# Optimization experiments

Hardware: AMD Instinct MI355X
Metric: run time of the kernel (lower is better)

Reference implementation:

```python
import jax, jax.numpy as jnp
import numpy as np

LN_EPS = 1e-5

def _mha(xq, xkv, in_w, in_b, out_w, out_b, n_heads):
    # torch nn.MultiheadAttention, batch_first=True, dropout=0
    B, S, d = xq.shape
    T = xkv.shape[1]
    dh = d // n_heads
    wq, wk, wv = jnp.split(in_w, 3, axis=0)   # each [d, d]
    bq, bk, bv = jnp.split(in_b, 3)
    q = (xq @ wq.T + bq).reshape(B, S, n_heads, dh).transpose(0, 2, 1, 3)
    k = (xkv @ wk.T + bk).reshape(B, T, n_heads, dh).transpose(0, 2, 1, 3)
    v = (xkv @ wv.T + bv).reshape(B, T, n_heads, dh).transpose(0, 2, 1, 3)
    scores = jnp.einsum('bhsd,bhtd->bhst', q, k) / jnp.sqrt(jnp.asarray(dh, xq.dtype))
    attn = jax.nn.softmax(scores, axis=-1)    # explicit [B,H,S,T] weights (need_weights=True path)
    o = jnp.einsum('bhst,bhtd->bhsd', attn, v)
    o = o.transpose(0, 2, 1, 3).reshape(B, S, d)
    return o @ out_w.T + out_b

def _ln(x, g, b):
    mu = jnp.mean(x, axis=-1, keepdims=True)
    var = jnp.mean(jnp.square(x - mu), axis=-1, keepdims=True)
    return (x - mu) / jnp.sqrt(var + LN_EPS) * g + b

def setup_inputs() -> dict:
    key = jax.random.key(0)
    B, S, T, d, ff = 4, 1024, 1024, 1024, 4096
    ks = jax.random.split(key, 10)
    s = 0.02
    return {
        'x': jax.random.normal(ks[0], (B, S, d), jnp.float32),
        'mem': jax.random.normal(ks[1], (B, T, d), jnp.float32),
        'sa_in_w': jax.random.normal(ks[2], (3 * d, d), jnp.float32) * s,
        'sa_in_b': jnp.zeros((3 * d,), jnp.float32),
        'sa_out_w': jax.random.normal(ks[3], (d, d), jnp.float32) * s,
        'sa_out_b': jnp.zeros((d,), jnp.float32),
        'ca_in_w': jax.random.normal(ks[4], (3 * d, d), jnp.float32) * s,
        'ca_in_b': jnp.zeros((3 * d,), jnp.float32),
        'ca_out_w': jax.random.normal(ks[5], (d, d), jnp.float32) * s,
        'ca_out_b': jnp.zeros((d,), jnp.float32),
        'ff_w1': jax.random.normal(ks[6], (ff, d), jnp.float32) * s,
        'ff_b1': jnp.zeros((ff,), jnp.float32),
        'ff_w2': jax.random.normal(ks[7], (d, ff), jnp.float32) * s,
        'ff_b2': jnp.zeros((d,), jnp.float32),
        'ln1_g': jnp.ones((d,), jnp.float32), 'ln1_b': jnp.zeros((d,), jnp.float32),
        'ln2_g': jnp.ones((d,), jnp.float32), 'ln2_b': jnp.zeros((d,), jnp.float32),
        'ln3_g': jnp.ones((d,), jnp.float32), 'ln3_b': jnp.zeros((d,), jnp.float32),
        'n_heads': 16,
    }

def reference(x, mem, sa_in_w, sa_in_b, sa_out_w, sa_out_b,
              ca_in_w, ca_in_b, ca_out_w, ca_out_b,
              ff_w1, ff_b1, ff_w2, ff_b2,
              ln1_g, ln1_b, ln2_g, ln2_b, ln3_g, ln3_b, n_heads):
    sa = _mha(x, x, sa_in_w, sa_in_b, sa_out_w, sa_out_b, n_heads)
    x = _ln(x + sa, ln1_g, ln1_b)
    ca = _mha(x, mem, ca_in_w, ca_in_b, ca_out_w, ca_out_b, n_heads)
    x = _ln(x + ca, ln2_g, ln2_b)
    h = jax.nn.gelu(x @ ff_w1.T + ff_b1, approximate=False)  # torch nn.GELU default = exact erf
    ff = h @ ff_w2.T + ff_b2
    return _ln(x + ff, ln3_g, ln3_b)
```

## Files before the change

kernel.cpp:

```cpp
#include <hip/hip_runtime.h>
#include <cstddef>

#define D_MODEL 1024
#define SEQ     1024
#define BATCH   4
#define NHEAD   16
#define DH      64
#define FFDIM   4096
#define NTOK    (BATCH*SEQ)

typedef float f32x4  __attribute__((ext_vector_type(4)));
typedef short bf16x8 __attribute__((ext_vector_type(8)));

static __device__ __forceinline__ unsigned short f2bf(float x){
  union { float f; unsigned u; } v; v.f = x;
  unsigned r = v.u + 0x7fffu + ((v.u >> 16) & 1u);
  return (unsigned short)(r >> 16);
}

static __device__ __forceinline__ float bf2f(unsigned short h){
  union { unsigned u; float f; } v; v.u = ((unsigned)h) << 16; return v.f;
}

static __device__ __forceinline__ void gl_lds16(const void* g, void* l){
  __builtin_amdgcn_global_load_lds((const __attribute__((address_space(1))) void*)g,
                                   (__attribute__((address_space(3))) void*)l, 16, 0, 0);
}

struct CvtJobs {
  const float* src[8];
  unsigned short* dst[8];
  int n[8];
};

__global__ __launch_bounds__(256) void cvt_kernel(CvtJobs jobs){
  int seg = blockIdx.y;
  const float* s = jobs.src[seg];
  unsigned short* d = jobs.dst[seg];
  int n = jobs.n[seg];
  int stride = gridDim.x * 256 * 4;
  for (int i = (blockIdx.x*256 + threadIdx.x)*4; i < n; i += stride){
    float4 v = *(const float4*)(s + i);
    ushort4 o;
    o.x = f2bf(v.x); o.y = f2bf(v.y); o.z = f2bf(v.z); o.w = f2bf(v.w);
    *(ushort4*)(d + i) = o;
  }
}

template<int EPI>
static __device__ __forceinline__ void gemm_core(
    unsigned short* smem,
    const unsigned short* __restrict__ A,
    const unsigned short* __restrict__ B,
    const float* __restrict__ bias,
    void* __restrict__ out0,
    unsigned short* __restrict__ vt,
    int N, int K, int kbeg, int kend, int row0, int col0)
{
  unsigned short* As = smem;
  unsigned short* Bs = smem + 128*64;
  const int tid  = threadIdx.x;
  const int w    = tid >> 6, lane = tid & 63;
  const int quad = lane >> 4, l15 = lane & 15;
  const int lr   = lane >> 3, lc = lane & 7;
  const int csrc = lc ^ lr;
  const int sw   = l15 & 7;
  const int wm = (w >> 1) * 64, wn = (w & 1) * 64;

  f32x4 acc[4][4];
  const f32x4 zero4 = {0.f, 0.f, 0.f, 0.f};
  #pragma unroll
  for (int i=0;i<4;i++)
    #pragma unroll
    for (int j=0;j<4;j++)
      acc[i][j] = zero4;

  const unsigned short* Ag = A + (size_t)(row0 + lr)*K + csrc*8;
  const unsigned short* Bg = B + (size_t)(col0 + lr)*K + csrc*8;

  for (int k0 = kbeg; k0 < kend; k0 += 64){
    #pragma unroll
    for (int i=0;i<4;i++){
      gl_lds16(Ag + (size_t)(i*32 + w*8)*K + k0, &As[i*2048 + w*512]);
      gl_lds16(Bg + (size_t)(i*32 + w*8)*K + k0, &Bs[i*2048 + w*512]);
    }
    __syncthreads();
    #pragma unroll
    for (int ks=0; ks<2; ks++){
      bf16x8 af[4], bfr[4];
      #pragma unroll
      for (int i=0;i<4;i++)
        af[i] = *(const bf16x8*)&As[(wm + i*16 + l15)*64 + ((ks*4 + quad) ^ sw)*8];
      #pragma unroll
      for (int j=0;j<4;j++)
        bfr[j] = *(const bf16x8*)&Bs[(wn + j*16 + l15)*64 + ((ks*4 + quad) ^ sw)*8];
      #pragma unroll
      for (int i=0;i<4;i++)
        #pragma unroll
        for (int j=0;j<4;j++)
          acc[i][j] = __builtin_amdgcn_mfma_f32_16x16x32_bf16(af[i], bfr[j], acc[i][j], 0, 0, 0);
    }
    __syncthreads();
  }

  float bj[4];
  #pragma unroll
  for (int j=0;j<4;j++) bj[j] = bias[col0 + wn + j*16 + l15];

  #pragma unroll
  for (int i=0;i<4;i++){
    #pragma unroll
    for (int r=0;r<4;r++){
      int row = row0 + wm + i*16 + quad*4 + r;
      #pragma unroll
      for (int j=0;j<4;j++){
        int col = col0 + wn + j*16 + l15;
        float v = acc[i][j][r] + bj[j];
        if (EPI == 2){
          float t = 0.7978845608f * (v + 0.044715f * v * v * v);
          float e = __expf(2.f * t);
          float th = 1.f - 2.f * __builtin_amdgcn_rcpf(e + 1.f);
          v = 0.5f * v * (1.f + th);
        }
        if (EPI == 0){
          ((float*)out0)[(size_t)row*N + col] = v;
        } else if (EPI == 1 || EPI == 2){
          ((unsigned short*)out0)[(size_t)row*N + col] = f2bf(v);
        } else if (EPI == 3){
          if (col < 2048) ((unsigned short*)out0)[(size_t)row*2048 + col] = f2bf(v);
          else {
            int h = (col - 2048) >> 6, d = col & 63;
            int b = row >> 10, t = row & 1023;
            vt[((size_t)(b*NHEAD + h)*DH + d)*SEQ + t] = f2bf(v);
          }
        } else {
          if (col < 1024) ((unsigned short*)out0)[(size_t)row*1024 + col] = f2bf(v);
          else {
            int h = (col - 1024) >> 6, d = col & 63;
            int b = row >> 10, t = row & 1023;
            vt[((size_t)(b*NHEAD + h)*DH + d)*SEQ + t] = f2bf(v);
          }
        }
      }
    }
  }
}

template<int EPI>
__global__ __launch_bounds__(256) void gemm_plain(
    const unsigned short* A, const unsigned short* B, const float* bias,
    void* out0, unsigned short* vt, int N, int K)
{
  __shared__ __align__(16) unsigned short smem[2*128*64];
  gemm_core<EPI>(smem, A, B, bias, out0, vt, N, K, 0, K,
                 blockIdx.y*128, blockIdx.x*128);
}

__global__ __launch_bounds__(256) void gemm_split(
    const unsigned short* A, const unsigned short* B, const float* bias,
    unsigned short* outA, unsigned short* outB, int N, int K)
{
  __shared__ __align__(16) unsigned short smem[2*128*64];
  int kseg = K >> 1;
  int kbeg = blockIdx.z * kseg;
  unsigned short* o = blockIdx.z ? outB : outA;
  gemm_core<1>(smem, A, B, bias, o, nullptr, N, K, kbeg, kbeg + kseg,
               blockIdx.y*128, blockIdx.x*128);
}

__global__ __launch_bounds__(256) void gemm_ca(
    const unsigned short* x1b, const unsigned short* memb,
    const unsigned short* w, const float* biasq, const float* biaskv,
    unsigned short* qout, unsigned short* kout, unsigned short* vt)
{
  __shared__ __align__(16) unsigned short smem[2*128*64];
  if (blockIdx.x < 8)
    gemm_core<1>(smem, x1b, w, biasq, qout, nullptr, 1024, 1024, 0, 1024,
                 blockIdx.y*128, blockIdx.x*128);
  else
    gemm_core<4>(smem, memb, w + (size_t)1024*1024, biaskv, kout, vt,
                 2048, 1024, 0, 1024, blockIdx.y*128, (blockIdx.x - 8)*128);
}

__global__ __launch_bounds__(256) void attn_kernel(
    const unsigned short* __restrict__ Q, int ldq,
    const unsigned short* __restrict__ Kp, int ldk,
    const unsigned short* __restrict__ Vt,
    unsigned short* __restrict__ O)
{
  __shared__ __align__(16) unsigned short Qs[128*64];
  __shared__ __align__(16) unsigned short Ks[64*64];
  __shared__ __align__(16) unsigned short Vs[64*64];
  __shared__ __align__(16) unsigned short Ps[4*32*72];

  const int tid  = threadIdx.x;
  const int w    = tid >> 6, lane = tid & 63;
  const int quad = lane >> 4, l15 = lane & 15;
  const int lr   = lane >> 3, lc = lane & 7;
  const int csrc = lc ^ lr;
  const int sw   = l15 & 7;
  const int q0   = blockIdx.x * 128;
  const int h = blockIdx.y, b = blockIdx.z;
  const int tok0 = b * SEQ;
  const int hoff = h * DH;
  const int bh   = b * NHEAD + h;

  #pragma unroll
  for (int i=0;i<4;i++){
    int r = i*32 + w*8 + lr;
    gl_lds16(Q + (size_t)(tok0 + q0 + r)*ldq + hoff + csrc*8, &Qs[i*2048 + w*512]);
  }
  __syncthreads();

  bf16x8 qb[2][2];
  #pragma unroll
  for (int qi=0;qi<2;qi++){
    int row = w*32 + qi*16 + l15;
    qb[qi][0] = *(const bf16x8*)&Qs[row*64 + ((0 + quad) ^ sw)*8];
    qb[qi][1] = *(const bf16x8*)&Qs[row*64 + ((4 + quad) ^ sw)*8];
  }

  float lsum[2] = {0.f, 0.f};
  f32x4 oacc[2][4];
  const f32x4 zero4 = {0.f, 0.f, 0.f, 0.f};
  #pragma unroll
  for (int qi=0;qi<2;qi++)
    #pragma unroll
    for (int dt=0;dt<4;dt++)
      oacc[qi][dt] = zero4;

  unsigned short* pw = &Ps[w*32*72];

  for (int kc = 0; kc < SEQ/64; ++kc){
    __syncthreads();
    #pragma unroll
    for (int i=0;i<2;i++){
      int r = i*32 + w*8 + lr;
      gl_lds16(Kp + (size_t)(tok0 + kc*64 + r)*ldk + hoff + csrc*8, &Ks[i*2048 + w*512]);
      gl_lds16(Vt + ((size_t)bh*DH + r)*SEQ + kc*64 + csrc*8,       &Vs[i*2048 + w*512]);
    }
    __syncthreads();

    #pragma unroll
    for (int tj=0;tj<4;tj++){
      bf16x8 ka0 = *(const bf16x8*)&Ks[(tj*16 + l15)*64 + ((0 + quad) ^ sw)*8];
      bf16x8 ka1 = *(const bf16x8*)&Ks[(tj*16 + l15)*64 + ((4 + quad) ^ sw)*8];
      #pragma unroll
      for (int qi=0;qi<2;qi++){
        f32x4 z = zero4;
        z = __builtin_amdgcn_mfma_f32_16x16x32_bf16(ka0, qb[qi][0], z, 0, 0, 0);
        z = __builtin_amdgcn_mfma_f32_16x16x32_bf16(ka1, qb[qi][1], z, 0, 0, 0);
        float p0 = __expf(z[0] * 0.125f);
        float p1 = __expf(z[1] * 0.125f);
        float p2 = __expf(z[2] * 0.125f);
        float p3 = __expf(z[3] * 0.125f);
        lsum[qi] += (p0 + p1) + (p2 + p3);
        short4 pk;
        pk.x = (short)f2bf(p0); pk.y = (short)f2bf(p1);
        pk.z = (short)f2bf(p2); pk.w = (short)f2bf(p3);
        *(short4*)&pw[(qi*16 + l15)*72 + tj*16 + quad*4] = pk;
      }
    }

    #pragma unroll
    for (int qi=0;qi<2;qi++){
      bf16x8 pa0 = *(const bf16x8*)&pw[(qi*16 + l15)*72 + quad*8];
      bf16x8 pa1 = *(const bf16x8*)&pw[(qi*16 + l15)*72 + 32 + quad*8];
      #pragma unroll
      for (int dt=0;dt<4;dt++){
        bf16x8 vb0 = *(const bf16x8*)&Vs[(dt*16 + l15)*64 + ((0 + quad) ^ sw)*8];
        bf16x8 vb1 = *(const bf16x8*)&Vs[(dt*16 + l15)*64 + ((4 + quad) ^ sw)*8];
        oacc[qi][dt] = __builtin_amdgcn_mfma_f32_16x16x32_bf16(pa0, vb0, oacc[qi][dt], 0, 0, 0);
        oacc[qi][dt] = __builtin_amdgcn_mfma_f32_16x16x32_bf16(pa1, vb1, oacc[qi][dt], 0, 0, 0);
      }
    }
  }

  #pragma unroll
  for (int qi=0;qi<2;qi++){
    lsum[qi] += __shfl_xor(lsum[qi], 16);
    lsum[qi] += __shfl_xor(lsum[qi], 32);
  }

  #pragma unroll
  for (int qi=0;qi<2;qi++){
    #pragma unroll
    for (int r=0;r<4;r++){
      float lv = __shfl(lsum[qi], quad*4 + r);
      float rinv = __builtin_amdgcn_rcpf(lv);
      size_t qrow = (size_t)(tok0 + q0 + w*32 + qi*16 + quad*4 + r);
      #pragma unroll
      for (int dt=0;dt<4;dt++)
        O[qrow*D_MODEL + hoff + dt*16 + l15] = f2bf(oacc[qi][dt][r] * rinv);
    }
  }
}

__global__ __launch_bounds__(256) void ln_kernel(
    const float* __restrict__ resid,
    const unsigned short* __restrict__ d1,
    const unsigned short* __restrict__ d2,
    const float* __restrict__ g, const float* __restrict__ beta,
    float* __restrict__ outf, unsigned short* __restrict__ outb)
{
  const int row = blockIdx.x;
  const int t = threadIdx.x;
  const size_t base = (size_t)row * D_MODEL;
  float4 a = *(const float4*)(resid + base + t*4);
  ushort4 p4 = *(const ushort4*)(d1 + base + t*4);
  ushort4 q4 = *(const ushort4*)(d2 + base + t*4);
  float v0 = a.x + bf2f(p4.x) + bf2f(q4.x);
  float v1 = a.y + bf2f(p4.y) + bf2f(q4.y);
  float v2 = a.z + bf2f(p4.z) + bf2f(q4.z);
  float v3 = a.w + bf2f(p4.w) + bf2f(q4.w);
  float s1 = v0+v1+v2+v3;
  float s2 = v0*v0+v1*v1+v2*v2+v3*v3;
  #pragma unroll
  for (int off=32; off>0; off>>=1){
    s1 += __shfl_down(s1, off);
    s2 += __shfl_down(s2, off);
  }
  __shared__ float red[8];
  const int wid = t >> 6;
  if ((t & 63) == 0){ red[wid*2] = s1; red[wid*2+1] = s2; }
  __syncthreads();
  s1 = red[0]+red[2]+red[4]+red[6];
  s2 = red[1]+red[3]+red[5]+red[7];
  float mean = s1 * (1.f/1024.f);
  float var  = s2 * (1.f/1024.f) - mean*mean;
  float rstd = rsqrtf(var + 1e-5f);
  float4 gg = *(const float4*)(g + t*4);
  float4 bb = *(const float4*)(beta + t*4);
  float y0 = (v0-mean)*rstd*gg.x + bb.x;
  float y1 = (v1-mean)*rstd*gg.y + bb.y;
  float y2 = (v2-mean)*rstd*gg.z + bb.z;
  float y3 = (v3-mean)*rstd*gg.w + bb.w;
  if (outf) *(float4*)(outf + base + t*4) = make_float4(y0,y1,y2,y3);
  if (outb){
    ushort4 o;
    o.x = f2bf(y0); o.y = f2bf(y1); o.z = f2bf(y2); o.w = f2bf(y3);
    *(ushort4*)(outb + base + t*4) = o;
  }
}

extern "C" void kernel_launch(void* const* d_in, const int* in_sizes, int n_in,
                              void* d_out, int out_size, void* d_ws, size_t ws_size,
                              hipStream_t stream)
{
  const float* x        = (const float*)d_in[0];
  const float* mem      = (const float*)d_in[1];
  const float* sa_in_w  = (const float*)d_in[2];
  const float* sa_in_b  = (const float*)d_in[3];
  const float* sa_out_w = (const float*)d_in[4];
  const float* sa_out_b = (const float*)d_in[5];
  const float* ca_in_w  = (const float*)d_in[6];
  const float* ca_in_b  = (const float*)d_in[7];
  const float* ca_out_w = (const float*)d_in[8];
  const float* ca_out_b = (const float*)d_in[9];
  const float* ff_w1    = (const float*)d_in[10];
  const float* ff_b1    = (const float*)d_in[11];
  const float* ff_w2    = (const float*)d_in[12];
  const float* ff_b2    = (const float*)d_in[13];
  const float* ln1_g    = (const float*)d_in[14];
  const float* ln1_b    = (const float*)d_in[15];
  const float* ln2_g    = (const float*)d_in[16];
  const float* ln2_b    = (const float*)d_in[17];
  const float* ln3_g    = (const float*)d_in[18];
  const float* ln3_b    = (const float*)d_in[19];

  char* base = (char*)d_ws;
  size_t off = 0;
  auto alloc = [&](size_t bytes) -> void* {
    void* r = base + off;
    off += (bytes + 255) & ~(size_t)255;
    return r;
  };
  unsigned short* xb     = (unsigned short*)alloc((size_t)NTOK*1024*2);
  unsigned short* memb   = (unsigned short*)alloc((size_t)NTOK*1024*2);
  unsigned short* wsain  = (unsigned short*)alloc((size_t)3072*1024*2);
  unsigned short* wsaout = (unsigned short*)alloc((size_t)1024*1024*2);
  unsigned short* wcain  = (unsigned short*)alloc((size_t)3072*1024*2);
  unsigned short* wcaout = (unsigned short*)alloc((size_t)1024*1024*2);
  unsigned short* wff1   = (unsigned short*)alloc((size_t)4096*1024*2);
  unsigned short* wff2   = (unsigned short*)alloc((size_t)4096*1024*2);
  unsigned short* qkvbuf = (unsigned short*)alloc((size_t)NTOK*3072*2);
  unsigned short* attnb  = (unsigned short*)alloc((size_t)NTOK*1024*2);
  float*          proj   = (float*)alloc((size_t)NTOK*1024*4);
  float*          x1f    = (float*)alloc((size_t)NTOK*1024*4);
  unsigned short* x1b    = (unsigned short*)alloc((size_t)NTOK*1024*2);
  float*          x2f    = (float*)alloc((size_t)NTOK*1024*4);
  unsigned short* x2b    = (unsigned short*)alloc((size_t)NTOK*1024*2);

  unsigned short* vt   = (unsigned short*)proj;
  unsigned short* hbuf = qkvbuf;
  unsigned short* pA   = (unsigned short*)proj;
  unsigned short* pB1  = (unsigned short*)x2f;
  unsigned short* pB2  = (unsigned short*)xb;
  unsigned short* pB3  = (unsigned short*)x1f;

  CvtJobs jobs;
  jobs.src[0]=x;        jobs.dst[0]=xb;     jobs.n[0]=NTOK*1024;
  jobs.src[1]=mem;      jobs.dst[1]=memb;   jobs.n[1]=NTOK*1024;
  jobs.src[2]=sa_in_w;  jobs.dst[2]=wsain;  jobs.n[2]=3072*1024;
  jobs.src[3]=sa_out_w; jobs.dst[3]=wsaout; jobs.n[3]=1024*1024;
  jobs.src[4]=ca_in_w;  jobs.dst[4]=wcain;  jobs.n[4]=3072*1024;
  jobs.src[5]=ca_out_w; jobs.dst[5]=wcaout; jobs.n[5]=1024*1024;
  jobs.src[6]=ff_w1;    jobs.dst[6]=wff1;   jobs.n[6]=4096*1024;
  jobs.src[7]=ff_w2;    jobs.dst[7]=wff2;   jobs.n[7]=4096*1024;
  cvt_kernel<<<dim3(1024,8), 256, 0, stream>>>(jobs);

  unsigned short* qk_sa = qkvbuf;
  gemm_plain<3><<<dim3(24,32), 256, 0, stream>>>(xb, wsain, sa_in_b, qk_sa, vt, 3072, 1024);
  attn_kernel<<<dim3(8,16,4), 256, 0, stream>>>(qk_sa, 2048, qk_sa + 1024, 2048, vt, attnb);
  gemm_split<<<dim3(8,32,2), 256, 0, stream>>>(attnb, wsaout, sa_out_b, pA, pB1, 1024, 1024);
  ln_kernel<<<NTOK, 256, 0, stream>>>(x, pA, pB1, ln1_g, ln1_b, x1f, x1b);

  unsigned short* qca  = qkvbuf;
  unsigned short* kbuf = qkvbuf + (size_t)NTOK*1024;
  gemm_ca<<<dim3(24,32), 256, 0, stream>>>(x1b, memb, wcain, ca_in_b, ca_in_b + 1024,
                                           qca, kbuf, vt);
  attn_kernel<<<dim3(8,16,4), 256, 0, stream>>>(qca, 1024, kbuf, 1024, vt, attnb);
  gemm_split<<<dim3(8,32,2), 256, 0, stream>>>(attnb, wcaout, ca_out_b, pA, pB2, 1024, 1024);
  ln_kernel<<<NTOK, 256, 0, stream>>>(x1f, pA, pB2, ln2_g, ln2_b, x2f, x2b);

  gemm_plain<2><<<dim3(32,32), 256, 0, stream>>>(x2b, wff1, ff_b1, hbuf, nullptr, 4096, 1024);
  gemm_split<<<dim3(8,32,2), 256, 0, stream>>>(hbuf, wff2, ff_b2, pA, pB3, 1024, 4096);
  ln_kernel<<<NTOK, 256, 0, stream>>>(x2f, pA, pB3, ln3_g, ln3_b, (float*)d_out, nullptr);
}
```

Measured before the change: 516.2 us.

## Swizzle GEMM and attention block order for XCD-aware L2 locality

Adds a block-index remapping that groups tiles by id&7, which matches how consecutive workgroups are spread over the 8 XCDs on MI355X, so each XCD works on a compact RX x RY region of the output. The remap is applied to all GEMM launches, and attention moves to a 1-D grid that keeps all q-tiles of a batch-head on the same XCD. The aim is more L2 reuse of A/B tiles and K/V per head. The two EPI variants are merged into one parameterized epilogue, and gemm_ca now runs a single code path whose branches depend on a runtime flag, which may add some register pressure or divergence.

Result: no change. 506.4 us (-1.9%).

```diff
diff --git a/kernel.cpp b/kernel.cpp
--- a/kernel.cpp
+++ b/kernel.cpp
@@ -25,6 +25,15 @@
 static __device__ __forceinline__ void gl_lds16(const void* g, void* l){
   __builtin_amdgcn_global_load_lds((const __attribute__((address_space(1))) void*)g,
                                    (__attribute__((address_space(3))) void*)l, 16, 0, 0);
+}
+
+static __device__ __forceinline__ int2 swz_tile(int gx, int RX, int RY){
+  int id = blockIdx.y * gx + blockIdx.x;
+  int x = id & 7, s = id >> 3;
+  int nrx = gx / RX;
+  int bx = (x % nrx) * RX + (s % RX);
+  int by = (x / nrx) * RY + (s / RX);
+  return make_int2(bx, by);
 }
 
 struct CvtJobs {
@@ -55,7 +64,8 @@
     const float* __restrict__ bias,
     void* __restrict__ out0,
     unsigned short* __restrict__ vt,
-    int N, int K, int kbeg, int kend, int row0, int col0)
+    int N, int K, int kbeg, int kend, int row0, int col0,
+    int split, int ldout)
 {
   unsigned short* As = smem;
   unsigned short* Bs = smem + 128*64;
@@ -126,17 +136,10 @@
           ((float*)out0)[(size_t)row*N + col] = v;
         } else if (EPI == 1 || EPI == 2){
           ((unsigned short*)out0)[(size_t)row*N + col] = f2bf(v);
-        } else if (EPI == 3){
-          if (col < 2048) ((unsigned short*)out0)[(size_t)row*2048 + col] = f2bf(v);
+        } else {
+          if (col < split) ((unsigned short*)out0)[(size_t)row*ldout + col] = f2bf(v);
           else {
-            int h = (col - 2048) >> 6, d = col & 63;
-            int b = row >> 10, t = row & 1023;
-            vt[((size_t)(b*NHEAD + h)*DH + d)*SEQ + t] = f2bf(v);
-          }
-        } else {
-          if (col < 1024) ((unsigned short*)out0)[(size_t)row*1024 + col] = f2bf(v);
-          else {
-            int h = (col - 1024) >> 6, d = col & 63;
+            int h = (col - split) >> 6, d = col & 63;
             int b = row >> 10, t = row & 1023;
             vt[((size_t)(b*NHEAD + h)*DH + d)*SEQ + t] = f2bf(v);
           }
@@ -147,13 +150,15 @@
 }
 
 template<int EPI>
-__global__ __launch_bounds__(256) void gemm_plain(
+__global__ __launch_bounds__(256) void gemm_swz(
     const unsigned short* A, const unsigned short* B, const float* bias,
-    void* out0, unsigned short* vt, int N, int K)
+    void* out0, unsigned short* vt, int N, int K, int split, int ldout,
+    int RX, int RY)
 {
   __shared__ __align__(16) unsigned short smem[2*128*64];
+  int2 t = swz_tile(gridDim.x, RX, RY);
   gemm_core<EPI>(smem, A, B, bias, out0, vt, N, K, 0, K,
-                 blockIdx.y*128, blockIdx.x*128);
+                 t.y*128, t.x*128, split, ldout);
 }
 
 __global__ __launch_bounds__(256) void gemm_split(
@@ -161,11 +166,12 @@
     unsigned short* outA, unsigned short* outB, int N, int K)
 {
   __shared__ __align__(16) unsigned short smem[2*128*64];
+  int2 t = swz_tile(gridDim.x, 4, 8);
   int kseg = K >> 1;
   int kbeg = blockIdx.z * kseg;
   unsigned short* o = blockIdx.z ? outB : outA;
   gemm_core<1>(smem, A, B, bias, o, nullptr, N, K, kbeg, kbeg + kseg,
-               blockIdx.y*128, blockIdx.x*128);
+               t.y*128, t.x*128, 0, 0);
 }
 
 __global__ __launch_bounds__(256) void gemm_ca(
@@ -174,12 +180,15 @@
     unsigned short* qout, unsigned short* kout, unsigned short* vt)
 {
   __shared__ __align__(16) unsigned short smem[2*128*64];
-  if (blockIdx.x < 8)
-    gemm_core<1>(smem, x1b, w, biasq, qout, nullptr, 1024, 1024, 0, 1024,
-                 blockIdx.y*128, blockIdx.x*128);
-  else
-    gemm_core<4>(smem, memb, w + (size_t)1024*1024, biaskv, kout, vt,
-                 2048, 1024, 0, 1024, blockIdx.y*128, (blockIdx.x - 8)*128);
+  int2 t = swz_tile(gridDim.x, 12, 8);
+  const bool qs = t.x < 8;
+  const unsigned short* A = qs ? x1b : memb;
+  const unsigned short* B = qs ? w : w + (size_t)1024*1024;
+  const float* bias       = qs ? biasq : biaskv;
+  unsigned short* out     = qs ? qout : kout;
+  const int col0          = qs ? t.x*128 : (t.x - 8)*128;
+  gemm_core<5>(smem, A, B, bias, out, vt, 2048, 1024, 0, 1024,
+               t.y*128, col0, 1024, 1024);
 }
 
 __global__ __launch_bounds__(256) void attn_kernel(
@@ -199,11 +208,13 @@
   const int lr   = lane >> 3, lc = lane & 7;
   const int csrc = lc ^ lr;
   const int sw   = l15 & 7;
-  const int q0   = blockIdx.x * 128;
-  const int h = blockIdx.y, b = blockIdx.z;
+  const int id = blockIdx.x;
+  const int xc = id & 7, s = id >> 3;
+  const int bh = xc*8 + (s >> 3), qt = s & 7;
+  const int b = bh >> 4, h = bh & 15;
+  const int q0   = qt * 128;
   const int tok0 = b * SEQ;
   const int hoff = h * DH;
-  const int bh   = b * NHEAD + h;
 
   #pragma unroll
   for (int i=0;i<4;i++){
@@ -410,8 +421,9 @@
   cvt_kernel<<<dim3(1024,8), 256, 0, stream>>>(jobs);
 
   unsigned short* qk_sa = qkvbuf;
-  gemm_plain<3><<<dim3(24,32), 256, 0, stream>>>(xb, wsain, sa_in_b, qk_sa, vt, 3072, 1024);
-  attn_kernel<<<dim3(8,16,4), 256, 0, stream>>>(qk_sa, 2048, qk_sa + 1024, 2048, vt, attnb);
+  gemm_swz<5><<<dim3(24,32), 256, 0, stream>>>(xb, wsain, sa_in_b, qk_sa, vt,
+                                               3072, 1024, 2048, 2048, 12, 8);
+  attn_kernel<<<512, 256, 0, stream>>>(qk_sa, 2048, qk_sa + 1024, 2048, vt, attnb);
   gemm_split<<<dim3(8,32,2), 256, 0, stream>>>(attnb, wsaout, sa_out_b, pA, pB1, 1024, 1024);
   ln_kernel<<<NTOK, 256, 0, stream>>>(x, pA, pB1, ln1_g, ln1_b, x1f, x1b);
 
@@ -419,11 +431,12 @@
   unsigned short* kbuf = qkvbuf + (size_t)NTOK*1024;
   gemm_ca<<<dim3(24,32), 256, 0, stream>>>(x1b, memb, wcain, ca_in_b, ca_in_b + 1024,
                                            qca, kbuf, vt);
-  attn_kernel<<<dim3(8,16,4), 256, 0, stream>>>(qca, 1024, kbuf, 1024, vt, attnb);
+  attn_kernel<<<512, 256, 0, stream>>>(qca, 1024, kbuf, 1024, vt, attnb);
   gemm_split<<<dim3(8,32,2), 256, 0, stream>>>(attnb, wcaout, ca_out_b, pA, pB2, 1024, 1024);
   ln_kernel<<<NTOK, 256, 0, stream>>>(x1f, pA, pB2, ln2_g, ln2_b, x2f, x2b);
 
-  gemm_plain<2><<<dim3(32,32), 256, 0, stream>>>(x2b, wff1, ff_b1, hbuf, nullptr, 4096, 1024);
+  gemm_swz<2><<<dim3(32,32), 256, 0, stream>>>(x2b, wff1, ff_b1, hbuf, nullptr,
+                                               4096, 1024, 0, 0, 8, 16);
   gemm_split<<<dim3(8,32,2), 256, 0, stream>>>(hbuf, wff2, ff_b2, pA, pB3, 1024, 4096);
   ln_kernel<<<NTOK, 256, 0, stream>>>(x2f, pA, pB3, ln3_g, ln3_b, (float*)d_out, nullptr);
 }
```
